# Optimization experiments

Hardware: AMD Instinct MI355X
Metric: run time of the kernel (lower is better)

Reference implementation:

```python
import jax, jax.numpy as jnp
import numpy as np

B, S, H, T = 64, 512, 768, 3


def setup_inputs() -> dict:
    key = jax.random.key(0)
    ks = jax.random.split(key, 8)
    hidden = jax.random.normal(ks[0], (B, S, H), dtype=jnp.float32)
    labels = jax.random.randint(ks[1], (B, S), 0, T, dtype=jnp.int32)
    # variable-length attention mask; torchcrf requires mask[:, 0] all on
    lengths = jax.random.randint(ks[2], (B,), S // 4, S + 1, dtype=jnp.int32)
    mask = (jnp.arange(S)[None, :] < lengths[:, None]).astype(jnp.int32)
    W = jax.random.normal(ks[3], (H, T), dtype=jnp.float32) * 0.02
    b = jax.random.normal(ks[4], (T,), dtype=jnp.float32) * 0.02
    transitions = jax.random.normal(ks[5], (T, T), dtype=jnp.float32) * 0.1
    start_trans = jax.random.normal(ks[6], (T,), dtype=jnp.float32) * 0.1
    end_trans = jax.random.normal(ks[7], (T,), dtype=jnp.float32) * 0.1
    return {"hidden": hidden, "labels": labels, "mask": mask, "W": W, "b": b,
            "transitions": transitions, "start_trans": start_trans, "end_trans": end_trans}


def _crf_nll(emissions, tags, mask, trans, start, end):
    # emissions: (B,S,T) float; tags/mask: (B,S) int. Returns sum NLL (scalar).
    mask_f = mask.astype(emissions.dtype)
    bidx = jnp.arange(emissions.shape[0])
    # --- numerator: score of the given tag path ---
    first_tag = tags[:, 0]
    num = start[first_tag] + emissions[bidx, 0, first_tag]
    prev, cur = tags[:, :-1], tags[:, 1:]
    step = trans[prev, cur] + jnp.take_along_axis(emissions[:, 1:], cur[..., None], axis=2)[..., 0]
    num = num + jnp.sum(step * mask_f[:, 1:], axis=1)
    lengths = jnp.sum(mask, axis=1)
    last_tag = jnp.take_along_axis(tags, (lengths - 1)[:, None], axis=1)[:, 0]
    num = num + end[last_tag]
    # --- denominator: log-partition via forward algorithm (lax.scan) ---
    alpha0 = start[None, :] + emissions[:, 0]  # (B,T)
    def fwd_step(alpha, inp):
        e, m = inp  # e: (B,T), m: (B,)
        nxt = jax.scipy.special.logsumexp(alpha[:, :, None] + trans[None] + e[:, None, :], axis=1)
        return jnp.where(m[:, None] > 0, nxt, alpha), None
    emis_t = jnp.swapaxes(emissions[:, 1:], 0, 1)  # (S-1,B,T)
    mask_t = jnp.swapaxes(mask[:, 1:], 0, 1)       # (S-1,B)
    alpha, _ = jax.lax.scan(fwd_step, alpha0, (emis_t, mask_t))
    logZ = jax.scipy.special.logsumexp(alpha + end[None, :], axis=1)
    return jnp.sum(logZ - num)


def reference(hidden, labels, mask, W, b, transitions, start_trans, end_trans):
    # classifier: Linear + ReLU -> emissions (B,S,T)
    emissions = jax.nn.relu(jnp.einsum("bsh,ht->bst", hidden, W) + b)
    negloglike = _crf_nll(emissions, labels, mask, transitions, start_trans, end_trans)
    return emissions, negloglike
```

## Files before the change

### kernel.cpp

```cpp
#include <hip/hip_runtime.h>
#include <math.h>

#define NB 64
#define NS 512
#define NH 768
#define NT 3
#define EMIS_N (NB * NS * NT)
#define NEGINF (-1e30f)
#define WPB 128
#define PSTRIDE 12

__device__ __forceinline__ float lse3(float a, float b, float c) {
    float m = fmaxf(fmaxf(a, b), c);
    return m + __logf(__expf(a - m) + __expf(b - m) + __expf(c - m));
}

__global__ __launch_bounds__(256) void emis_crf_kernel(
    const float* __restrict__ hidden,
    const int*   __restrict__ labels,
    const int*   __restrict__ mask,
    const float* __restrict__ W,
    const float* __restrict__ bias,
    const float* __restrict__ trans,
    const float* __restrict__ startv,
    float* __restrict__ out,
    float* __restrict__ ws)
{
    if (blockIdx.x == 0 && threadIdx.x == 0) out[EMIS_N] = 0.0f;

    const int lane = threadIdx.x & 63;
    const int wid  = blockIdx.x * 4 + (threadIdx.x >> 6);
    const int sub  = lane & 15;
    const int rsel = lane >> 4;
    const int row  = wid * 4 + rsel;
    const int b    = wid >> 7;
    const int w    = wid & 127;
    const int p    = (w << 2) + rsel;

    const float* hrow = hidden + (size_t)row * NH;

    float a0 = 0.f, a1 = 0.f, a2 = 0.f;
    #pragma unroll
    for (int it = 0; it < 12; ++it) {
        const int h0 = it * 64 + sub * 4;
        const float4 x  = *reinterpret_cast<const float4*>(hrow + h0);
        const float4 q0 = *reinterpret_cast<const float4*>(W + h0 * 3);
        const float4 q1 = *reinterpret_cast<const float4*>(W + h0 * 3 + 4);
        const float4 q2 = *reinterpret_cast<const float4*>(W + h0 * 3 + 8);
        a0 = fmaf(x.x, q0.x, a0); a1 = fmaf(x.x, q0.y, a1); a2 = fmaf(x.x, q0.z, a2);
        a0 = fmaf(x.y, q0.w, a0); a1 = fmaf(x.y, q1.x, a1); a2 = fmaf(x.y, q1.y, a2);
        a0 = fmaf(x.z, q1.z, a0); a1 = fmaf(x.z, q1.w, a1); a2 = fmaf(x.z, q2.x, a2);
        a0 = fmaf(x.w, q2.y, a0); a1 = fmaf(x.w, q2.z, a1); a2 = fmaf(x.w, q2.w, a2);
    }
    #pragma unroll
    for (int d = 8; d; d >>= 1) {
        a0 += __shfl_xor(a0, d);
        a1 += __shfl_xor(a1, d);
        a2 += __shfl_xor(a2, d);
    }

    const float e0 = fmaxf(a0 + bias[0], 0.f);
    const float e1 = fmaxf(a1 + bias[1], 0.f);
    const float e2 = fmaxf(a2 + bias[2], 0.f);

    if (sub < 3) out[row * NT + sub] = (sub == 0) ? e0 : (sub == 1) ? e1 : e2;

    const int* lrow = labels + b * NS;
    const int* mrow = mask   + b * NS;
    int   mk = 0;
    float term = 0.f;
    if (sub == 0) {
        mk = mrow[p];
        const int labc = lrow[p];
        const float esel = (labc == 0) ? e0 : (labc == 1) ? e1 : e2;
        if (p == 0) {
            term = startv[labc] + esel;
        } else if (mk) {
            const int labp = lrow[p - 1];
            term = trans[labp * 3 + labc] + esel;
        }
    }

    const int il = (lane < 9) ? (lane / 3) : 0;
    const int jl = (lane < 9) ? (lane % 3) : 0;
    const float tc0 = trans[jl], tc1 = trans[3 + jl], tc2 = trans[6 + jl];
    float Pv = (il == jl) ? 0.f : NEGINF;

    #pragma unroll
    for (int k = 0; k < 4; ++k) {
        const int src = k << 4;
        const float ee0 = __shfl(e0, src);
        const float ee1 = __shfl(e1, src);
        const float ee2 = __shfl(e2, src);
        const int   mm  = __shfl(mk, src);
        const float Pi0 = __shfl(Pv, il * 3 + 0);
        const float Pi1 = __shfl(Pv, il * 3 + 1);
        const float Pi2 = __shfl(Pv, il * 3 + 2);
        const float ej  = (jl == 0) ? ee0 : (jl == 1) ? ee1 : ee2;
        const float q   = lse3(Pi0 + tc0, Pi1 + tc1, Pi2 + tc2) + ej;
        const bool act  = (((w << 2) + k) >= 1) && (mm != 0);
        Pv = act ? q : Pv;
    }

    const float np = __shfl(term, 0) + __shfl(term, 16) +
                     __shfl(term, 32) + __shfl(term, 48);

    float* wp = ws + wid * PSTRIDE;
    if (lane < 9) wp[lane] = Pv;
    if (lane == 0) wp[9] = np;
}

__global__ __launch_bounds__(64) void crf_combine(
    const float* __restrict__ emis,
    const int*   __restrict__ labels,
    const int*   __restrict__ mask,
    const float* __restrict__ startv,
    const float* __restrict__ endv,
    const float* __restrict__ ws,
    float* __restrict__ nll)
{
    const int b    = blockIdx.x;
    const int lane = threadIdx.x;
    const int* mrow = mask   + b * NS;
    const int* lrow = labels + b * NS;

    int lsum = 0;
    #pragma unroll
    for (int k = 0; k < 8; ++k) lsum += mrow[lane + k * 64];
    #pragma unroll
    for (int d = 32; d; d >>= 1) lsum += __shfl_xor(lsum, d);
    const int len = lsum;

    const float* base = ws + (size_t)b * WPB * PSTRIDE;
    const float* pa = base + (2 * lane)     * PSTRIDE;
    const float* pb = base + (2 * lane + 1) * PSTRIDE;
    float A[9], Bm[9];
    #pragma unroll
    for (int i = 0; i < 9; ++i) A[i]  = pa[i];
    #pragma unroll
    for (int i = 0; i < 9; ++i) Bm[i] = pb[i];
    float np = pa[9] + pb[9];

    float P[9];
    #pragma unroll
    for (int i = 0; i < 3; ++i)
        #pragma unroll
        for (int j = 0; j < 3; ++j)
            P[i * 3 + j] = lse3(A[i * 3 + 0] + Bm[0 + j],
                                A[i * 3 + 1] + Bm[3 + j],
                                A[i * 3 + 2] + Bm[6 + j]);

    #pragma unroll
    for (int d = 1; d < 64; d <<= 1) {
        float Q[9];
        #pragma unroll
        for (int i = 0; i < 9; ++i) Q[i] = __shfl_down(P[i], d);
        const bool valid = (lane + d) < 64;
        float R[9];
        #pragma unroll
        for (int i = 0; i < 3; ++i)
            #pragma unroll
            for (int j = 0; j < 3; ++j)
                R[i * 3 + j] = lse3(P[i * 3 + 0] + Q[0 + j],
                                    P[i * 3 + 1] + Q[3 + j],
                                    P[i * 3 + 2] + Q[6 + j]);
        #pragma unroll
        for (int i = 0; i < 9; ++i) P[i] = valid ? R[i] : P[i];
    }

    #pragma unroll
    for (int d = 32; d; d >>= 1) np += __shfl_xor(np, d);

    if (lane == 0) {
        const float* erow = emis + (size_t)b * NS * NT;
        const float a0 = startv[0] + erow[0];
        const float a1 = startv[1] + erow[1];
        const float a2 = startv[2] + erow[2];
        const float f0 = lse3(a0 + P[0], a1 + P[3], a2 + P[6]);
        const float f1 = lse3(a0 + P[1], a1 + P[4], a2 + P[7]);
        const float f2 = lse3(a0 + P[2], a1 + P[5], a2 + P[8]);
        const float logZ = lse3(f0 + endv[0], f1 + endv[1], f2 + endv[2]);

        const int tl = lrow[len - 1];
        const float num = np + endv[tl];
        atomicAdd(nll, logZ - num);
    }
}

extern "C" void kernel_launch(void* const* d_in, const int* in_sizes, int n_in,
                              void* d_out, int out_size, void* d_ws, size_t ws_size,
                              hipStream_t stream) {
    const float* hidden = (const float*)d_in[0];
    const int*   labels = (const int*)  d_in[1];
    const int*   maskp  = (const int*)  d_in[2];
    const float* W      = (const float*)d_in[3];
    const float* bias   = (const float*)d_in[4];
    const float* trans  = (const float*)d_in[5];
    const float* startv = (const float*)d_in[6];
    const float* endv   = (const float*)d_in[7];
    float* out = (float*)d_out;
    float* ws  = (float*)d_ws;

    emis_crf_kernel<<<2048, 256, 0, stream>>>(hidden, labels, maskp, W, bias,
                                              trans, startv, out, ws);
    crf_combine<<<NB, 64, 0, stream>>>(out, labels, maskp, startv, endv, ws,
                                       out + EMIS_N);
}
```

Before: 28.86 us.

## Stage hidden rows and W into LDS via async global_load_lds

Each block now copies its 16 hidden rows and the whole W matrix into shared memory using direct global-to-LDS loads, waits on them, and then runs the dot products from LDS. Before, each lane read hidden and W straight from global memory with float4 loads. The aim is fully coalesced wide transfers and no repeated W fetches per lane. The cost is about 57KB of LDS per block, which limits occupancy, plus a full drain of outstanding loads before any compute starts, so transfers no longer overlap with arithmetic.

Result: slower. 34.36 us (+19.1%).

```diff
diff --git a/kernel.cpp b/kernel.cpp
--- a/kernel.cpp
+++ b/kernel.cpp
@@ -9,6 +9,10 @@
 #define NEGINF (-1e30f)
 #define WPB 128
 #define PSTRIDE 12
+#define RPB 16
+
+typedef __attribute__((address_space(1))) const void glob_void;
+typedef __attribute__((address_space(3))) void lds_void;
 
 __device__ __forceinline__ float lse3(float a, float b, float c) {
     float m = fmaxf(fmaxf(a, b), c);
@@ -26,27 +30,56 @@
     float* __restrict__ out,
     float* __restrict__ ws)
 {
-    if (blockIdx.x == 0 && threadIdx.x == 0) out[EMIS_N] = 0.0f;
-
-    const int lane = threadIdx.x & 63;
-    const int wid  = blockIdx.x * 4 + (threadIdx.x >> 6);
+    __shared__ alignas(16) float tile[RPB * NH];
+    __shared__ alignas(16) float wlds[NH * NT];
+
+    const int tid  = threadIdx.x;
+    const int lane = tid & 63;
+    const int wv   = tid >> 6;
+    const int blk  = blockIdx.x;
+    const int row0 = blk * RPB;
+
+    if (blk == 0 && tid == 0) out[EMIS_N] = 0.0f;
+
+    #pragma unroll
+    for (int k = 0; k < 3; ++k) {
+        const int c = k * 256 + tid;
+        if (c < (NH * NT) / 4) {
+            __builtin_amdgcn_global_load_lds(
+                (glob_void*)(W + (size_t)c * 4),
+                (lds_void*)(wlds + (k * 256 + wv * 64) * 4),
+                16, 0, 0);
+        }
+    }
+
+    const float* hbase = hidden + (size_t)row0 * NH;
+    #pragma unroll
+    for (int i = 0; i < 12; ++i) {
+        const int cf = (wv * 12 + i) * 256;
+        __builtin_amdgcn_global_load_lds(
+            (glob_void*)(hbase + cf + lane * 4),
+            (lds_void*)(tile + cf),
+            16, 0, 0);
+    }
+
+    asm volatile("s_waitcnt vmcnt(0)" ::: "memory");
+    __syncthreads();
+
     const int sub  = lane & 15;
     const int rsel = lane >> 4;
-    const int row  = wid * 4 + rsel;
-    const int b    = wid >> 7;
-    const int w    = wid & 127;
-    const int p    = (w << 2) + rsel;
-
-    const float* hrow = hidden + (size_t)row * NH;
+    const int lr   = wv * 4 + rsel;
+    const int row  = row0 + lr;
+    const int b    = row >> 9;
+    const int p    = row & (NS - 1);
 
     float a0 = 0.f, a1 = 0.f, a2 = 0.f;
     #pragma unroll
     for (int it = 0; it < 12; ++it) {
         const int h0 = it * 64 + sub * 4;
-        const float4 x  = *reinterpret_cast<const float4*>(hrow + h0);
-        const float4 q0 = *reinterpret_cast<const float4*>(W + h0 * 3);
-        const float4 q1 = *reinterpret_cast<const float4*>(W + h0 * 3 + 4);
-        const float4 q2 = *reinterpret_cast<const float4*>(W + h0 * 3 + 8);
+        const float4 x  = *reinterpret_cast<const float4*>(tile + lr * NH + h0);
+        const float4 q0 = *reinterpret_cast<const float4*>(wlds + h0 * 3);
+        const float4 q1 = *reinterpret_cast<const float4*>(wlds + h0 * 3 + 4);
+        const float4 q2 = *reinterpret_cast<const float4*>(wlds + h0 * 3 + 8);
         a0 = fmaf(x.x, q0.x, a0); a1 = fmaf(x.x, q0.y, a1); a2 = fmaf(x.x, q0.z, a2);
         a0 = fmaf(x.y, q0.w, a0); a1 = fmaf(x.y, q1.x, a1); a2 = fmaf(x.y, q1.y, a2);
         a0 = fmaf(x.z, q1.z, a0); a1 = fmaf(x.z, q1.w, a1); a2 = fmaf(x.z, q2.x, a2);
@@ -86,6 +119,7 @@
     const float tc0 = trans[jl], tc1 = trans[3 + jl], tc2 = trans[6 + jl];
     float Pv = (il == jl) ? 0.f : NEGINF;
 
+    const int pbase = p & ~3;
     #pragma unroll
     for (int k = 0; k < 4; ++k) {
         const int src = k << 4;
@@ -98,13 +132,14 @@
         const float Pi2 = __shfl(Pv, il * 3 + 2);
         const float ej  = (jl == 0) ? ee0 : (jl == 1) ? ee1 : ee2;
         const float q   = lse3(Pi0 + tc0, Pi1 + tc1, Pi2 + tc2) + ej;
-        const bool act  = (((w << 2) + k) >= 1) && (mm != 0);
+        const bool act  = ((pbase + k) >= 1) && (mm != 0);
         Pv = act ? q : Pv;
     }
 
     const float np = __shfl(term, 0) + __shfl(term, 16) +
                      __shfl(term, 32) + __shfl(term, 48);
 
+    const int wid = blk * 4 + wv;
     float* wp = ws + wid * PSTRIDE;
     if (lane < 9) wp[lane] = Pv;
     if (lane == 0) wp[9] = np;
```
